# Performance work log

Measured on AMD Instinct MI355X. Metric: run time of the kernel, lower is better.

The kernel has to match this reference:

```python
import jax, jax.numpy as jnp
import numpy as np

DIM = 2048
NUM_HEADS = 8
HEAD_DIM = DIM // NUM_HEADS  # 256; forward requires seq_len == HEAD_DIM
B = 64
N = HEAD_DIM  # q @ k (untransposed) only works when N == head_dim


def setup_inputs() -> dict:
    key = jax.random.key(0)
    k1, k2, k3, k4 = jax.random.split(key, 4)
    x = jax.random.normal(k1, (B, N, DIM), dtype=jnp.float32)
    # torch Linear stores weight as [out_features, in_features]
    w_qkv = jax.random.normal(k2, (3 * DIM, DIM), dtype=jnp.float32) * 0.02
    w_proj = jax.random.normal(k3, (DIM, DIM), dtype=jnp.float32) * 0.02
    b_proj = jax.random.normal(k4, (DIM,), dtype=jnp.float32) * 0.02
    return {"x": x, "w_qkv": w_qkv, "w_proj": w_proj, "b_proj": b_proj}


def reference(x, w_qkv, w_proj, b_proj):
    Bb, Nn, C = x.shape
    H, D = NUM_HEADS, C // NUM_HEADS
    # qkv projection (no bias), split into q,k,v of shape [B,H,N,D]
    qkv = (x @ w_qkv.T).reshape(Bb, Nn, 3, H, D).transpose(2, 0, 3, 1, 4)
    q, k, v = qkv[0], qkv[1], qkv[2]
    # NON-standard: q @ k with k NOT transposed -> contracts q's feature dim
    # against k's token dim (valid because D == N). attn: [B,H,N,N]
    attn = jnp.matmul(q, k)
    # transpose last two dims, then softmax over the new last axis
    attn = jnp.swapaxes(attn, -2, -1)
    attn = jax.nn.softmax(attn, axis=-1)
    out = jnp.matmul(attn, v)              # [B,H,N,D]
    out = out.swapaxes(1, 2).reshape(Bb, Nn, C)
    return out @ w_proj.T + b_proj
```

## Files before the change

kernel.cpp:

```cpp
#include <hip/hip_runtime.h>
#include <hip/hip_bf16.h>

typedef unsigned short u16;
typedef __attribute__((ext_vector_type(4))) float f32x4;
typedef __attribute__((ext_vector_type(8))) short short8;
typedef __attribute__((ext_vector_type(8))) u16 us8;


__device__ __forceinline__ u16 f2bf(float f) {
  union { float f; unsigned u; } v; v.f = f;
  unsigned r = v.u + 0x7fffu + ((v.u >> 16) & 1u);
  return (u16)(r >> 16);
}
__device__ __forceinline__ float bf2f(u16 h) {
  union { unsigned u; float f; } v; v.u = ((unsigned)h) << 16; return v.f;
}

__global__ void beacon_kernel(float* __restrict__ out, float val, int n) {
  int stride = gridDim.x * blockDim.x;
  for (int i = blockIdx.x * blockDim.x + threadIdx.x; i < n; i += stride)
    out[i] = val;
}

__global__ void split_kernel(const float* __restrict__ in, u16* __restrict__ hi,
                             u16* __restrict__ lo, int n4) {
  int stride = gridDim.x * blockDim.x;
  for (int i = blockIdx.x * blockDim.x + threadIdx.x; i < n4; i += stride) {
    f32x4 v = ((const f32x4*)in)[i];
    ushort4 h;
    h.x = f2bf(v[0]); h.y = f2bf(v[1]); h.z = f2bf(v[2]); h.w = f2bf(v[3]);
    ((ushort4*)hi)[i] = h;
    if (lo) {
      ushort4 l;
      l.x = f2bf(v[0] - bf2f(h.x)); l.y = f2bf(v[1] - bf2f(h.y));
      l.z = f2bf(v[2] - bf2f(h.z)); l.w = f2bf(v[3] - bf2f(h.w));
      ((ushort4*)lo)[i] = l;
    }
  }
}

#define SCHED0 __builtin_amdgcn_sched_barrier(0)
#define LGKM0 do { asm volatile("s_waitcnt lgkmcnt(0)" ::: "memory"); SCHED0; } while (0)
#define VM0 do { asm volatile("s_waitcnt vmcnt(0)" ::: "memory"); } while (0)
#define BAR __builtin_amdgcn_s_barrier()

template<int EPI>
__global__ __launch_bounds__(512, 2)
void gemm256(const u16* __restrict__ A0, const u16* __restrict__ A1,
             const u16* __restrict__ B0, const u16* __restrict__ B1,
             int ldA, int ldB, int ntiles, int segShift, int gridMx,
             u16* __restrict__ qh, u16* __restrict__ ql,
             u16* __restrict__ kh, u16* __restrict__ kl,
             u16* __restrict__ vv,
             float* __restrict__ fout, const float* __restrict__ bias) {
  extern __shared__ __align__(16) u16 lds[];

  const int tid = threadIdx.x;
  const int w = tid >> 6, lane = tid & 63;
  const int wr = w >> 2, wcn = w & 3;
  const int l15 = lane & 15, g = lane >> 4;
  const int rsw = l15 & 7;
  const int scol = (((tid & 7) ^ ((tid >> 3) & 7)) << 3);

  int bid = blockIdx.x, cpx = gridDim.x >> 3;
  int swz = (bid & 7) * cpx + (bid >> 3);
  int m0 = (swz % gridMx) << 8;
  int n0 = (swz / gridMx) << 8;

  const u16* As[2] = {A0, A1};
  const u16* Bs[2] = {B0, B1};
  const int kmask = (1 << segShift) - 1;

  f32x4 acc[8][4] = {};
  short8 af[8], bA[4], bB[4];

  auto stageA = [&](int db, const u16* Ab, int k0) {
    #pragma unroll
    for (int s = 0; s < 4; ++s) {
      const u16* src = Ab + (size_t)(m0 + s * 64 + (tid >> 3)) * ldA + k0 + scol;
      u16* dst = lds + db * 32768 + s * 4096 + tid * 8;
      __builtin_amdgcn_global_load_lds(
          (const __attribute__((address_space(1))) unsigned*)src,
          (__attribute__((address_space(3))) unsigned*)dst, 16, 0, 0);
    }
  };
  auto stageB = [&](int db, const u16* Bb, int k0) {
    #pragma unroll
    for (int s = 0; s < 4; ++s) {
      const u16* src = Bb + (size_t)(n0 + s * 64 + (tid >> 3)) * ldB + k0 + scol;
      u16* dst = lds + db * 32768 + 16384 + s * 4096 + tid * 8;
      __builtin_amdgcn_global_load_lds(
          (const __attribute__((address_space(1))) unsigned*)src,
          (__attribute__((address_space(3))) unsigned*)dst, 16, 0, 0);
    }
  };
  auto readA = [&](int db, int MH) {
    #pragma unroll
    for (int f = 0; f < 4; ++f) {
      int row = wr * 128 + MH * 64 + f * 16 + l15;
      #pragma unroll
      for (int kk = 0; kk < 2; ++kk) {
        int sl = (kk * 4 + g) ^ rsw;
        af[f * 2 + kk] = *(const short8*)(lds + db * 32768 + row * 64 + sl * 8);
      }
    }
  };
  auto readB = [&](short8* bf, int db, int NH) {
    #pragma unroll
    for (int f = 0; f < 2; ++f) {
      int row = wcn * 64 + NH * 32 + f * 16 + l15;
      #pragma unroll
      for (int kk = 0; kk < 2; ++kk) {
        int sl = (kk * 4 + g) ^ rsw;
        bf[f * 2 + kk] = *(const short8*)(lds + db * 32768 + 16384 + row * 64 + sl * 8);
      }
    }
  };

#define MMA_QUAD(MH, NH, BF)                                                   \
  __builtin_amdgcn_s_setprio(1);                                               \
  _Pragma("unroll") for (int f = 0; f < 4; ++f)                                \
    _Pragma("unroll") for (int j = 0; j < 2; ++j)                              \
      _Pragma("unroll") for (int kk = 0; kk < 2; ++kk)                         \
        acc[(MH) * 4 + f][(NH) * 2 + j] =                                      \
            __builtin_amdgcn_mfma_f32_16x16x32_bf16(                           \
                af[f * 2 + kk], BF[j * 2 + kk],                                \
                acc[(MH) * 4 + f][(NH) * 2 + j], 0, 0, 0);                     \
  __builtin_amdgcn_s_setprio(0)

  const int T = ntiles;
  stageA(0, As[0], 0);
  stageB(0, Bs[0], 0);
  VM0;
  BAR; SCHED0;

  for (int t = 0; t < T - 1; ++t) {
    int cur = t & 1, nxt = cur ^ 1;
    int t1 = t + 1;
    const u16* An = As[t1 >> segShift];
    const u16* Bn = Bs[t1 >> segShift];
    int kn = (t1 & kmask) << 6;
    readA(cur, 0);
    readB(bA, cur, 0);
    stageA(nxt, An, kn);
    BAR; LGKM0;
    MMA_QUAD(0, 0, bA);
    BAR; SCHED0;
    readB(bB, cur, 1);
    stageB(nxt, Bn, kn);
    BAR; LGKM0;
    MMA_QUAD(0, 1, bB);
    BAR; SCHED0;
    readA(cur, 1);
    BAR; LGKM0;
    MMA_QUAD(1, 1, bB);
    BAR; SCHED0;
    MMA_QUAD(1, 0, bA);
    VM0;
    BAR; SCHED0;
  }
  {
    int cur = (T - 1) & 1;
    readA(cur, 0);
    readB(bA, cur, 0);
    LGKM0;
    MMA_QUAD(0, 0, bA);
    readB(bB, cur, 1);
    LGKM0;
    MMA_QUAD(0, 1, bB);
    readA(cur, 1);
    LGKM0;
    MMA_QUAD(1, 1, bB);
    MMA_QUAD(1, 0, bA);
  }
#undef MMA_QUAD

  #pragma unroll
  for (int i = 0; i < 8; ++i)
    #pragma unroll
    for (int j = 0; j < 4; ++j)
      #pragma unroll
      for (int rr = 0; rr < 4; ++rr) {
        int gm = m0 + wr * 128 + i * 16 + g * 4 + rr;
        int gn = n0 + wcn * 64 + j * 16 + l15;
        float val = acc[i][j][rr];
        if constexpr (EPI == 0) {
          int b = gm >> 8, tok = gm & 255;
          int sel = gn >> 11, head = (gn >> 8) & 7, col = gn & 255;
          size_t addr = (((size_t)b * 8 + head) * 256 + tok) * 256 + col;
          u16 h = f2bf(val), lo = f2bf(val - bf2f(h));
          if (sel == 0) { qh[addr] = h; ql[addr] = lo; }
          else          { kh[addr] = h; kl[addr] = lo; }
        } else if constexpr (EPI == 1) {
          int b = gm >> 8, tok = gm & 255;
          int head = (gn >> 8) & 7, col = gn & 255;
          size_t addr = (((size_t)b * 8 + head) * 256 + tok) * 256 + col;
          vv[addr] = f2bf(val);
        } else {
          fout[(size_t)gm * 2048 + gn] = val + bias[gn];
        }
      }
}

__global__ __launch_bounds__(256)
void fused_attn(const u16* __restrict__ kh, const u16* __restrict__ kl,
                const u16* __restrict__ qh, const u16* __restrict__ ql,
                const u16* __restrict__ vT, u16* __restrict__ aout) {
  __shared__ __align__(16) u16 sA[2048];
  __shared__ __align__(16) u16 sB[8192];
  __shared__ __align__(16) u16 sP[64 * 276];

  const int tid = threadIdx.x;
  const int wave = tid >> 6, lane = tid & 63;
  const int l15 = lane & 15, l16 = lane >> 4;
  const int sxor = (l15 >> 1) & 3;
  const int scol = ((lane & 3) ^ ((lane >> 3) & 3)) * 8;
  const int m0 = blockIdx.x << 6;
  const size_t zo = (size_t)blockIdx.y * 65536;
  const u16* As[3] = {kh + zo, kh + zo, kl + zo};
  const u16* Bs[3] = {qh + zo, ql + zo, qh + zo};

  f32x4 acc[16] = {};
  for (int ks = 0; ks < 24; ++ks) {
    int seg = ks >> 3, k0 = (ks & 7) * 32;
    {
      const u16* gp = As[seg];
      int chunk = wave;
      int r = chunk * 16 + (lane >> 2);
      const u16* src = gp + (size_t)(m0 + r) * 256 + k0 + scol;
      __builtin_amdgcn_global_load_lds(
          (const __attribute__((address_space(1))) unsigned*)src,
          (__attribute__((address_space(3))) unsigned*)(sA + chunk * 512), 16, 0, 0);
    }
    {
      const u16* gp = Bs[seg];
      #pragma unroll
      for (int c = 0; c < 4; ++c) {
        int chunk = wave + c * 4;
        int r = chunk * 16 + (lane >> 2);
        const u16* src = gp + (size_t)r * 256 + k0 + scol;
        __builtin_amdgcn_global_load_lds(
            (const __attribute__((address_space(1))) unsigned*)src,
            (__attribute__((address_space(3))) unsigned*)(sB + chunk * 512), 16, 0, 0);
      }
    }
    __syncthreads();

    short8 a;
    {
      int ra = (wave * 16 + l15) * 4 + (l16 ^ sxor);
      a = ((const short8*)sA)[ra];
    }
    #pragma unroll
    for (int c = 0; c < 16; ++c) {
      int rb = (c * 16 + l15) * 4 + (l16 ^ sxor);
      short8 b = ((const short8*)sB)[rb];
      acc[c] = __builtin_amdgcn_mfma_f32_16x16x32_bf16(a, b, acc[c], 0, 0, 0);
    }
    __syncthreads();
  }

  #pragma unroll
  for (int rr = 0; rr < 4; ++rr) {
    float m = acc[0][rr];
    #pragma unroll
    for (int c = 1; c < 16; ++c) m = fmaxf(m, acc[c][rr]);
    #pragma unroll
    for (int sh = 1; sh < 16; sh <<= 1) m = fmaxf(m, __shfl_xor(m, sh));
    float e[16];
    float s = 0.f;
    #pragma unroll
    for (int c = 0; c < 16; ++c) { e[c] = __expf(acc[c][rr] - m); s += e[c]; }
    #pragma unroll
    for (int sh = 1; sh < 16; sh <<= 1) s += __shfl_xor(s, sh);
    float inv = 1.0f / s;
    int prow = wave * 16 + l16 * 4 + rr;
    #pragma unroll
    for (int c = 0; c < 16; ++c)
      sP[prow * 276 + c * 16 + l15] = f2bf(e[c] * inv);
  }
  __syncthreads();

  const int wr2 = wave >> 1, wc2 = wave & 1;
  f32x4 acc2[2][8] = {};
  for (int ks = 0; ks < 8; ++ks) {
    int k0 = ks * 32;
    {
      #pragma unroll
      for (int c = 0; c < 4; ++c) {
        int chunk = wave + c * 4;
        int r = chunk * 16 + (lane >> 2);
        const u16* src = vT + zo + (size_t)r * 256 + k0 + scol;
        __builtin_amdgcn_global_load_lds(
            (const __attribute__((address_space(1))) unsigned*)src,
            (__attribute__((address_space(3))) unsigned*)(sB + chunk * 512), 16, 0, 0);
      }
    }
    __syncthreads();

    short8 a[2], b[8];
    #pragma unroll
    for (int i = 0; i < 2; ++i) {
      int prow = wr2 * 32 + i * 16 + l15;
      a[i] = *(const short8*)(sP + prow * 276 + k0 + l16 * 8);
    }
    #pragma unroll
    for (int j = 0; j < 8; ++j) {
      int rb = ((wc2 * 128 + j * 16 + l15)) * 4 + (l16 ^ sxor);
      b[j] = ((const short8*)sB)[rb];
    }
    #pragma unroll
    for (int i = 0; i < 2; ++i)
      #pragma unroll
      for (int j = 0; j < 8; ++j)
        acc2[i][j] = __builtin_amdgcn_mfma_f32_16x16x32_bf16(a[i], b[j], acc2[i][j], 0, 0, 0);
    __syncthreads();
  }

  int plane = blockIdx.y;
  #pragma unroll
  for (int i = 0; i < 2; ++i)
    #pragma unroll
    for (int j = 0; j < 8; ++j)
      #pragma unroll
      for (int rr = 0; rr < 4; ++rr) {
        int gi = m0 + wr2 * 32 + i * 16 + l16 * 4 + rr;
        int gd = wc2 * 128 + j * 16 + l15;
        size_t row = (size_t)(plane >> 3) * 256 + gi;
        size_t col = (size_t)(plane & 7) * 256 + gd;
        aout[row * 2048 + col] = f2bf(acc2[i][j][rr]);
      }
}

__global__ void transpose_inplace(u16* __restrict__ kh, u16* __restrict__ kl,
                                  u16* __restrict__ v) {
  __shared__ u16 ta[64][66], tb[64][66];
  u16* base = (blockIdx.z == 0) ? kh : (blockIdx.z == 1) ? kl : v;
  u16* pl = base + (size_t)blockIdx.y * 65536;
  const int RA[10] = {0,1,2,3, 0,0,0,1,1,2};
  const int CA[10] = {0,1,2,3, 1,2,3,2,3,3};
  int p = blockIdx.x;
  int R = RA[p], C = CA[p];
  bool diag = (R == C);
  int tid = threadIdx.x;
  int r = tid >> 2, c0 = (tid & 3) * 16;

  const us8* sa = (const us8*)(pl + (size_t)(R * 64 + r) * 256 + C * 64 + c0);
  us8 a0 = sa[0], a1 = sa[1];
  #pragma unroll
  for (int s = 0; s < 8; ++s) { ta[r][c0 + s] = a0[s]; ta[r][c0 + 8 + s] = a1[s]; }
  if (!diag) {
    const us8* sb = (const us8*)(pl + (size_t)(C * 64 + r) * 256 + R * 64 + c0);
    us8 b0 = sb[0], b1 = sb[1];
    #pragma unroll
    for (int s = 0; s < 8; ++s) { tb[r][c0 + s] = b0[s]; tb[r][c0 + 8 + s] = b1[s]; }
  }
  __syncthreads();
  us8 o0, o1;
  #pragma unroll
  for (int s = 0; s < 8; ++s) { o0[s] = ta[c0 + s][r]; o1[s] = ta[c0 + 8 + s][r]; }
  us8* da = (us8*)(pl + (size_t)(C * 64 + r) * 256 + R * 64 + c0);
  da[0] = o0; da[1] = o1;
  if (!diag) {
    us8 p0, p1;
    #pragma unroll
    for (int s = 0; s < 8; ++s) { p0[s] = tb[c0 + s][r]; p1[s] = tb[c0 + 8 + s][r]; }
    us8* db = (us8*)(pl + (size_t)(R * 64 + r) * 256 + C * 64 + c0);
    db[0] = p0; db[1] = p1;
  }
}

extern "C" void kernel_launch(void* const* d_in, const int* in_sizes, int n_in,
                              void* d_out, int out_size, void* d_ws, size_t ws_size,
                              hipStream_t stream) {
  const float* x  = (const float*)d_in[0];
  const float* wq = (const float*)d_in[1];
  const float* wp = (const float*)d_in[2];
  const float* bp = (const float*)d_in[3];
  float* out = (float*)d_out;
  char* ws = (char*)d_ws;

  const size_t MB = 1ull << 20;
  const size_t NEED = 432 * MB;
  if (ws_size < NEED) {
    beacon_kernel<<<2048, 256, 0, stream>>>(out, (float)(ws_size >> 20), 16384 * 2048);
    return;
  }

  u16* q_hi = (u16*)(ws);
  u16* q_lo = (u16*)(ws + 64 * MB);
  u16* k_hi = (u16*)(ws + 128 * MB);
  u16* k_lo = (u16*)(ws + 192 * MB);
  u16* vbuf = (u16*)(ws + 256 * MB);
  u16* x_hi = (u16*)(ws + 320 * MB);
  u16* w_hi = (u16*)(ws + 384 * MB);
  u16* w_lo = (u16*)(ws + 408 * MB);
  u16* attn = (u16*)(ws + 320 * MB);
  u16* wpb  = (u16*)(ws + 384 * MB);

  split_kernel<<<8192, 256, 0, stream>>>(x,  x_hi, nullptr, 16384 * 2048 / 4);
  split_kernel<<<4096, 256, 0, stream>>>(wq, w_hi, w_lo, 6144 * 2048 / 4);

  gemm256<0><<<1024, 512, 131072, stream>>>(
      x_hi, x_hi, w_hi, w_lo, 2048, 2048, 64, 5, 64,
      q_hi, q_lo, k_hi, k_lo, nullptr, nullptr, nullptr);
  const u16* wv = w_hi + (size_t)4096 * 2048;
  gemm256<1><<<512, 512, 131072, stream>>>(
      x_hi, x_hi, wv, wv, 2048, 2048, 32, 5, 64,
      nullptr, nullptr, nullptr, nullptr, vbuf, nullptr, nullptr);

  transpose_inplace<<<dim3(10, 512, 3), 256, 0, stream>>>(k_hi, k_lo, vbuf);

  fused_attn<<<dim3(4, 512), 256, 0, stream>>>(k_hi, k_lo, q_hi, q_lo, vbuf, attn);

  split_kernel<<<2048, 256, 0, stream>>>(wp, wpb, nullptr, 2048 * 2048 / 4);
  gemm256<2><<<512, 512, 131072, stream>>>(
      attn, attn, wpb, wpb, 2048, 2048, 32, 5, 64,
      nullptr, nullptr, nullptr, nullptr, nullptr, out, bp);
}
```

Before: 1.072 ms.

## Double-buffer LDS staging in fused attention and remap blocks for XCD locality

Adds double-buffered LDS tiles in both matmul phases of the fused attention kernel, so global-to-LDS loads for the next k-step are issued before the MFMAs of the current step. It also flattens the grid to 1D and remaps block ids so the four m-tiles of the same head plane are grouped, likely to improve L2 sharing across chiplets. The cost is more LDS per block, which may reduce occupancy. The code depends on VM0/BAR/LGKM0/SCHED0 macros assumed to be defined elsewhere.

```diff
diff --git a/kernel.cpp b/kernel.cpp
--- a/kernel.cpp
+++ b/kernel.cpp
@@ -206,8 +206,8 @@
 void fused_attn(const u16* __restrict__ kh, const u16* __restrict__ kl,
                 const u16* __restrict__ qh, const u16* __restrict__ ql,
                 const u16* __restrict__ vT, u16* __restrict__ aout) {
-  __shared__ __align__(16) u16 sA[2048];
-  __shared__ __align__(16) u16 sB[8192];
+  __shared__ __align__(16) u16 sA[2][2048];
+  __shared__ __align__(16) u16 sB[2][8192];
   __shared__ __align__(16) u16 sP[64 * 276];
 
   const int tid = threadIdx.x;
@@ -215,22 +215,24 @@
   const int l15 = lane & 15, l16 = lane >> 4;
   const int sxor = (l15 >> 1) & 3;
   const int scol = ((lane & 3) ^ ((lane >> 3) & 3)) * 8;
-  const int m0 = blockIdx.x << 6;
-  const size_t zo = (size_t)blockIdx.y * 65536;
+
+  const int bid = blockIdx.x;
+  const int plane = (bid & 7) * 64 + (bid >> 5);
+  const int mtile = (bid >> 3) & 3;
+  const int m0 = mtile << 6;
+  const size_t zo = (size_t)plane * 65536;
   const u16* As[3] = {kh + zo, kh + zo, kl + zo};
   const u16* Bs[3] = {qh + zo, ql + zo, qh + zo};
 
-  f32x4 acc[16] = {};
-  for (int ks = 0; ks < 24; ++ks) {
+  auto stageL = [&](int db, int ks) {
     int seg = ks >> 3, k0 = (ks & 7) * 32;
     {
       const u16* gp = As[seg];
-      int chunk = wave;
-      int r = chunk * 16 + (lane >> 2);
+      int r = wave * 16 + (lane >> 2);
       const u16* src = gp + (size_t)(m0 + r) * 256 + k0 + scol;
       __builtin_amdgcn_global_load_lds(
           (const __attribute__((address_space(1))) unsigned*)src,
-          (__attribute__((address_space(3))) unsigned*)(sA + chunk * 512), 16, 0, 0);
+          (__attribute__((address_space(3))) unsigned*)(sA[db] + wave * 512), 16, 0, 0);
     }
     {
       const u16* gp = Bs[seg];
@@ -241,23 +243,34 @@
         const u16* src = gp + (size_t)r * 256 + k0 + scol;
         __builtin_amdgcn_global_load_lds(
             (const __attribute__((address_space(1))) unsigned*)src,
-            (__attribute__((address_space(3))) unsigned*)(sB + chunk * 512), 16, 0, 0);
+            (__attribute__((address_space(3))) unsigned*)(sB[db] + chunk * 512), 16, 0, 0);
       }
     }
-    __syncthreads();
-
+  };
+
+  f32x4 acc[16] = {};
+  stageL(0, 0);
+  VM0; BAR; SCHED0;
+  for (int ks = 0; ks < 24; ++ks) {
+    int cur = ks & 1, nxt = cur ^ 1;
     short8 a;
     {
       int ra = (wave * 16 + l15) * 4 + (l16 ^ sxor);
-      a = ((const short8*)sA)[ra];
-    }
+      a = ((const short8*)sA[cur])[ra];
+    }
+    short8 b[16];
     #pragma unroll
     for (int c = 0; c < 16; ++c) {
       int rb = (c * 16 + l15) * 4 + (l16 ^ sxor);
-      short8 b = ((const short8*)sB)[rb];
-      acc[c] = __builtin_amdgcn_mfma_f32_16x16x32_bf16(a, b, acc[c], 0, 0, 0);
-    }
-    __syncthreads();
+      b[c] = ((const short8*)sB[cur])[rb];
+    }
+    if (ks < 23) stageL(nxt, ks + 1);
+    BAR; LGKM0;
+    #pragma unroll
+    for (int c = 0; c < 16; ++c)
+      acc[c] = __builtin_amdgcn_mfma_f32_16x16x32_bf16(a, b[c], acc[c], 0, 0, 0);
+    if (ks < 23) VM0;
+    BAR; SCHED0;
   }
 
   #pragma unroll
@@ -282,22 +295,24 @@
   __syncthreads();
 
   const int wr2 = wave >> 1, wc2 = wave & 1;
+  auto stageV = [&](int db, int ks) {
+    int k0 = ks * 32;
+    #pragma unroll
+    for (int c = 0; c < 4; ++c) {
+      int chunk = wave + c * 4;
+      int r = chunk * 16 + (lane >> 2);
+      const u16* src = vT + zo + (size_t)r * 256 + k0 + scol;
+      __builtin_amdgcn_global_load_lds(
+          (const __attribute__((address_space(1))) unsigned*)src,
+          (__attribute__((address_space(3))) unsigned*)(sB[db] + chunk * 512), 16, 0, 0);
+    }
+  };
   f32x4 acc2[2][8] = {};
+  stageV(0, 0);
+  VM0; BAR; SCHED0;
   for (int ks = 0; ks < 8; ++ks) {
+    int cur = ks & 1, nxt = cur ^ 1;
     int k0 = ks * 32;
-    {
-      #pragma unroll
-      for (int c = 0; c < 4; ++c) {
-        int chunk = wave + c * 4;
-        int r = chunk * 16 + (lane >> 2);
-        const u16* src = vT + zo + (size_t)r * 256 + k0 + scol;
-        __builtin_amdgcn_global_load_lds(
-            (const __attribute__((address_space(1))) unsigned*)src,
-            (__attribute__((address_space(3))) unsigned*)(sB + chunk * 512), 16, 0, 0);
-      }
-    }
-    __syncthreads();
-
     short8 a[2], b[8];
     #pragma unroll
     for (int i = 0; i < 2; ++i) {
@@ -306,18 +321,20 @@
     }
     #pragma unroll
     for (int j = 0; j < 8; ++j) {
-      int rb = ((wc2 * 128 + j * 16 + l15)) * 4 + (l16 ^ sxor);
-      b[j] = ((const short8*)sB)[rb];
-    }
+      int rb = (wc2 * 128 + j * 16 + l15) * 4 + (l16 ^ sxor);
+      b[j] = ((const short8*)sB[cur])[rb];
+    }
+    if (ks < 7) stageV(nxt, ks + 1);
+    BAR; LGKM0;
     #pragma unroll
     for (int i = 0; i < 2; ++i)
       #pragma unroll
       for (int j = 0; j < 8; ++j)
         acc2[i][j] = __builtin_amdgcn_mfma_f32_16x16x32_bf16(a[i], b[j], acc2[i][j], 0, 0, 0);
-    __syncthreads();
-  }
-
-  int plane = blockIdx.y;
+    if (ks < 7) VM0;
+    BAR; SCHED0;
+  }
+
   #pragma unroll
   for (int i = 0; i < 2; ++i)
     #pragma unroll
@@ -411,7 +428,7 @@
 
   transpose_inplace<<<dim3(10, 512, 3), 256, 0, stream>>>(k_hi, k_lo, vbuf);
 
-  fused_attn<<<dim3(4, 512), 256, 0, stream>>>(k_hi, k_lo, q_hi, q_lo, vbuf, attn);
+  fused_attn<<<2048, 256, 0, stream>>>(k_hi, k_lo, q_hi, q_lo, vbuf, attn);
 
   split_kernel<<<2048, 256, 0, stream>>>(wp, wpb, nullptr, 2048 * 2048 / 4);
   gemm256<2><<<512, 512, 131072, stream>>>(
```

Measured after the change: 1.076 ms. No clear change (+0.4%).
